# Optimization experiments

Hardware: AMD Instinct MI355X
Metric: run time of the kernel (lower is better)

The kernel has to match this reference:

```python
import jax, jax.numpy as jnp
import numpy as np

# NF4 codebook used by bitsandbytes Linear4bit (quant_type='nf4')
NF4_CODE = jnp.array([
    -1.0, -0.6961928009986877, -0.5250730514526367, -0.39491748809814453,
    -0.28444138169288635, -0.18477343022823334, -0.09105003625154495, 0.0,
    0.07958029955625534, 0.16093020141124725, 0.24611230194568634,
    0.33791524171829224, 0.44070982933044434, 0.5626170039176941,
    0.7229568362236023, 1.0], dtype=jnp.float32)

SCALE = 32.0 / 16.0  # alpha / r


def setup_inputs() -> dict:
    key = jax.random.key(0)
    k1, k2, k3, k4, k5 = jax.random.split(key, 5)
    B, S, IN, OUT, R = 4, 2048, 4096, 4096, 16
    BLK = 64  # Linear4bit default blocksize
    x = jax.random.normal(k1, (B, S, IN), dtype=jnp.float32)
    w_codes = jax.random.randint(k2, (OUT, IN), 0, 16, dtype=jnp.int32)
    absmax = jax.random.uniform(k3, (OUT, IN // BLK), dtype=jnp.float32)
    W_a = jax.random.normal(k4, (IN, R), dtype=jnp.float32)
    W_b = jax.random.normal(k5, (R, OUT), dtype=jnp.float32)
    return {"x": x, "w_codes": w_codes, "absmax": absmax, "W_a": W_a, "W_b": W_b}


def reference(x, w_codes, absmax, W_a, W_b):
    out_f, in_f = w_codes.shape
    blocks = absmax.shape[1]
    # NF4 dequantize: codebook lookup * per-block absmax scale  -> W [out, in]
    W = (NF4_CODE[w_codes].reshape(out_f, blocks, -1)
         * absmax[:, :, None]).reshape(out_f, in_f).astype(x.dtype)
    # quantized linear (no bias)
    y = jnp.einsum('bsi,oi->bso', x, W)
    # LoRA low-rank update: scale * (x @ W_a @ W_b)
    y = y + SCALE * ((x @ W_a.astype(x.dtype)) @ W_b.astype(x.dtype))
    return y
```

## Files before the change

### kernel.cpp

```cpp
#include <hip/hip_runtime.h>
#include <hip/hip_bf16.h>
#include <stdint.h>

#define IN_F 4096
#define OUT_F 4096
#define RANK 16
#define LORA_SCALE 2.0f

typedef __attribute__((ext_vector_type(8))) short short8;
typedef __attribute__((ext_vector_type(4))) float f32x4;
typedef __attribute__((ext_vector_type(16))) float f32x16;

__device__ __constant__ float NF4_CODE[16] = {
    -1.0f, -0.6961928009986877f, -0.5250730514526367f, -0.39491748809814453f,
    -0.28444138169288635f, -0.18477343022823334f, -0.09105003625154495f, 0.0f,
    0.07958029955625534f, 0.16093020141124725f, 0.24611230194568634f,
    0.33791524171829224f, 0.44070982933044434f, 0.5626170039176941f,
    0.7229568362236023f, 1.0f};

__device__ __forceinline__ short bf16_rne(float f) {
    uint32_t u = __builtin_bit_cast(uint32_t, f);
    u += 0x7fffu + ((u >> 16) & 1u);
    return (short)(u >> 16);
}

__device__ __forceinline__ void load_lds16(const short* g, short* l) {
    __builtin_amdgcn_global_load_lds(
        (const __attribute__((address_space(1))) void*)g,
        (__attribute__((address_space(3))) void*)l, 16, 0, 0);
}

__global__ __launch_bounds__(256)
void prep_kernel(const int* __restrict__ codes, const float* __restrict__ am,
                 const float* __restrict__ Wa, const float* __restrict__ Wb,
                 const float* __restrict__ x, short* __restrict__ Weff,
                 short* __restrict__ xb)
{
    const int tid = threadIdx.x;

    if (blockIdx.x >= 4096) {
        const size_t i = (size_t)(blockIdx.x - 4096) * 256 + tid;
        const f32x4* xv = (const f32x4*)x;
        f32x4 a = xv[2 * i], b = xv[2 * i + 1];
        short8 o;
        o[0] = bf16_rne(a[0]); o[1] = bf16_rne(a[1]);
        o[2] = bf16_rne(a[2]); o[3] = bf16_rne(a[3]);
        o[4] = bf16_rne(b[0]); o[5] = bf16_rne(b[1]);
        o[6] = bf16_rne(b[2]); o[7] = bf16_rne(b[3]);
        ((short8*)xb)[i] = o;
        return;
    }

    __shared__ float WaT[RANK * 64];
    __shared__ float Wbs[RANK * 64];

    const int iBase = (blockIdx.x & 63) * 64;
    const int oBase = (blockIdx.x >> 6) * 64;

    {
        f32x4 v = *(const f32x4*)(Wa + (size_t)iBase * RANK + tid * 4);
        #pragma unroll
        for (int j = 0; j < 4; j++) {
            int e = tid * 4 + j;
            WaT[(e & 15) * 64 + (e >> 4)] = v[j];
        }
        int r = tid >> 4, c = (tid & 15) * 4;
        f32x4 w = *(const f32x4*)(Wb + (size_t)r * OUT_F + oBase + c);
        *(f32x4*)&Wbs[r * 64 + c] = w;
    }
    __syncthreads();

    #pragma unroll
    for (int p = 0; p < 2; p++) {
        const int g  = tid + p * 256;
        const int o  = g >> 3;
        const int ig = (g & 7) * 8;
        const float amax = am[(size_t)(oBase + o) * (IN_F / 64) + (iBase >> 6)];

        const int4* cp = (const int4*)(codes + (size_t)(oBase + o) * IN_F + iBase + ig);
        int4 c0 = cp[0], c1 = cp[1];
        int cc[8] = {c0.x, c0.y, c0.z, c0.w, c1.x, c1.y, c1.z, c1.w};

        float acc[8] = {0, 0, 0, 0, 0, 0, 0, 0};
        #pragma unroll
        for (int r = 0; r < RANK; r++) {
            float wb = Wbs[r * 64 + o];
            f32x4 a0 = *(const f32x4*)&WaT[r * 64 + ig];
            f32x4 a1 = *(const f32x4*)&WaT[r * 64 + ig + 4];
            acc[0] += a0[0] * wb;  acc[1] += a0[1] * wb;
            acc[2] += a0[2] * wb;  acc[3] += a0[3] * wb;
            acc[4] += a1[0] * wb;  acc[5] += a1[1] * wb;
            acc[6] += a1[2] * wb;  acc[7] += a1[3] * wb;
        }

        short8 out;
        #pragma unroll
        for (int j = 0; j < 8; j++)
            out[j] = bf16_rne(NF4_CODE[cc[j] & 15] * amax + LORA_SCALE * acc[j]);
        *(short8*)(Weff + (size_t)(oBase + o) * IN_F + iBase + ig) = out;
    }
}

template<bool ABF16>
__global__ __launch_bounds__(256)
void gemm32(const void* __restrict__ Ain, const short* __restrict__ Bt,
            float* __restrict__ C)
{
    __shared__ __align__(16) short lds[16384];
    short* sA = lds;
    short* sB = lds + 8192;

    const int tid  = threadIdx.x;
    const int lane = tid & 63;
    const int wave = tid >> 6;
    const int mBase = blockIdx.y * 128;
    const int nBase = blockIdx.x * 128;
    const int wm = (wave >> 1) * 64;
    const int wn = (wave & 1) * 64;

    const int srow = tid >> 3;
    const int scol = ((tid & 7) ^ (srow & 7)) * 8;

    const short* gA[4]; const float* fA[4]; const short* gB[4];
    #pragma unroll
    for (int p = 0; p < 4; p++) {
        if constexpr (ABF16)
            gA[p] = (const short*)Ain + (size_t)(mBase + p * 32 + srow) * IN_F + scol;
        else
            fA[p] = (const float*)Ain + (size_t)(mBase + p * 32 + srow) * IN_F + scol;
        gB[p] = Bt + (size_t)(nBase + p * 32 + srow) * IN_F + scol;
    }
    short* dA[4]; short* dB[4];
    #pragma unroll
    for (int p = 0; p < 4; p++) {
        dA[p] = sA + (p * 256 + tid) * 8;
        dB[p] = sB + (p * 256 + tid) * 8;
    }

    const int l31 = lane & 31;
    const int h   = lane >> 5;
    const int r7  = lane & 7;
    int xo[4];
    #pragma unroll
    for (int s = 0; s < 4; s++) xo[s] = ((s * 2 + h) ^ r7) * 8;
    const int rA0 = (wm + l31) * 64, rA1 = rA0 + 32 * 64;
    const int rB0 = (wn + l31) * 64, rB1 = rB0 + 32 * 64;

    f32x16 acc[2][2];
    #pragma unroll
    for (int i = 0; i < 2; i++)
        #pragma unroll
        for (int j = 0; j < 2; j++)
            #pragma unroll
            for (int r = 0; r < 16; r++)
                acc[i][j][r] = 0.f;

    for (int k0 = 0; k0 < IN_F; k0 += 64) {
        if constexpr (ABF16) {
            #pragma unroll
            for (int p = 0; p < 4; p++) load_lds16(gA[p] + k0, dA[p]);
        } else {
            #pragma unroll
            for (int p = 0; p < 4; p++) {
                const float* s0 = fA[p] + k0;
                f32x4 v0 = *(const f32x4*)s0;
                f32x4 v1 = *(const f32x4*)(s0 + 4);
                short8 o;
                #pragma unroll
                for (int j = 0; j < 4; j++) {
                    o[j] = bf16_rne(v0[j]); o[j + 4] = bf16_rne(v1[j]);
                }
                *(short8*)dA[p] = o;
            }
        }
        #pragma unroll
        for (int p = 0; p < 4; p++) load_lds16(gB[p] + k0, dB[p]);
        __syncthreads();

        #pragma unroll
        for (int s = 0; s < 4; s++) {
            short8 a0 = *(const short8*)(sA + rA0 + xo[s]);
            short8 a1 = *(const short8*)(sA + rA1 + xo[s]);
            short8 b0 = *(const short8*)(sB + rB0 + xo[s]);
            short8 b1 = *(const short8*)(sB + rB1 + xo[s]);
            acc[0][0] = __builtin_amdgcn_mfma_f32_32x32x16_bf16(a0, b0, acc[0][0], 0, 0, 0);
            acc[0][1] = __builtin_amdgcn_mfma_f32_32x32x16_bf16(a0, b1, acc[0][1], 0, 0, 0);
            acc[1][0] = __builtin_amdgcn_mfma_f32_32x32x16_bf16(a1, b0, acc[1][0], 0, 0, 0);
            acc[1][1] = __builtin_amdgcn_mfma_f32_32x32x16_bf16(a1, b1, acc[1][1], 0, 0, 0);
        }
        __syncthreads();
    }

    #pragma unroll
    for (int mi = 0; mi < 2; mi++) {
        #pragma unroll
        for (int ni = 0; ni < 2; ni++) {
            const int col  = nBase + wn + ni * 32 + l31;
            const int rowb = mBase + wm + mi * 32 + 4 * h;
            #pragma unroll
            for (int r = 0; r < 16; r++) {
                const int row = rowb + (r & 3) + 8 * (r >> 2);
                C[(size_t)row * OUT_F + col] = acc[mi][ni][r];
            }
        }
    }
}

#define FENCE() __builtin_amdgcn_sched_barrier(0)
#define BARRIER() do { asm volatile("" ::: "memory"); FENCE(); \
    __builtin_amdgcn_s_barrier(); FENCE(); asm volatile("" ::: "memory"); } while(0)
#define WAIT_LGKM0() do { asm volatile("s_waitcnt lgkmcnt(0)" ::: "memory"); FENCE(); } while(0)
#define WAIT_VM6() do { asm volatile("s_waitcnt vmcnt(6)" ::: "memory"); FENCE(); } while(0)

#define STAGE_A(BUF, H, T) do { \
    const short* _g = gA + (size_t)(H) * 128 * IN_F + (T) * 64; \
    load_lds16(_g,                   lds + (BUF)*32768 + (H)*8192 + tid*8); \
    load_lds16(_g + (size_t)64*IN_F, lds + (BUF)*32768 + (H)*8192 + 4096 + tid*8); \
} while(0)

#define STAGE_B(BUF, H, T) do { \
    const short* _g = gB + (size_t)(H) * 128 * IN_F + (T) * 64; \
    load_lds16(_g,                   lds + (BUF)*32768 + 16384 + (H)*8192 + tid*8); \
    load_lds16(_g + (size_t)64*IN_F, lds + (BUF)*32768 + 16384 + (H)*8192 + 4096 + tid*8); \
} while(0)

#define READ_A(BUF, MQ) do { \
    const short* _s = lds + (BUF)*32768 + (MQ)*8192; \
    _Pragma("unroll") \
    for (int mf = 0; mf < 4; ++mf) { \
        const int row = wm*64 + mf*16 + l15; \
        const short* _r = _s + row*64; \
        const int rs = row & 7; \
        afr[mf][0] = *(const short8*)(_r + ((kl     ) ^ rs) * 8); \
        afr[mf][1] = *(const short8*)(_r + ((kl | 4) ^ rs) * 8); \
    } \
} while(0)

#define READ_B(BUF, NQ) do { \
    const short* _s = lds + (BUF)*32768 + 16384 + (NQ)*8192; \
    _Pragma("unroll") \
    for (int nf = 0; nf < 2; ++nf) { \
        const int row = wn*32 + nf*16 + l15; \
        const short* _r = _s + row*64; \
        const int rs = row & 7; \
        bfr[nf][0] = *(const short8*)(_r + ((kl     ) ^ rs) * 8); \
        bfr[nf][1] = *(const short8*)(_r + ((kl | 4) ^ rs) * 8); \
    } \
} while(0)

#define MFMA_QUAD(MQ, NQ) do { \
    _Pragma("unroll") \
    for (int ks = 0; ks < 2; ++ks) \
    _Pragma("unroll") \
    for (int mf = 0; mf < 4; ++mf) \
    _Pragma("unroll") \
    for (int nf = 0; nf < 2; ++nf) \
        acc[MQ][NQ][mf][nf] = __builtin_amdgcn_mfma_f32_16x16x32_bf16( \
            afr[mf][ks], bfr[nf][ks], acc[MQ][NQ][mf][nf], 0, 0, 0); \
} while(0)

#define PHASE(RDA, RDB, BUF, MQ, NQ, STAGE_STMT, VM_STMT) do { \
    if (RDA) READ_A(BUF, MQ); \
    if (RDB) READ_B(BUF, NQ); \
    STAGE_STMT; \
    BARRIER(); \
    WAIT_LGKM0(); \
    __builtin_amdgcn_s_setprio(1); \
    MFMA_QUAD(MQ, NQ); \
    __builtin_amdgcn_s_setprio(0); \
    VM_STMT; \
    BARRIER(); \
} while(0)

__global__ __launch_bounds__(512, 2)
void gemm256(const short* __restrict__ A, const short* __restrict__ Bt,
             float* __restrict__ C)
{
    __shared__ __align__(16) short lds[65536];

    const int tid  = threadIdx.x;
    const int lane = tid & 63;
    const int wave = tid >> 6;
    const int wm  = wave >> 2;
    const int wn  = wave & 3;
    const int l15 = lane & 15;
    const int kl  = lane >> 4;

    const int nwg = gridDim.x;
    int bid = blockIdx.x;
    bid = (bid & 7) * (nwg >> 3) + (bid >> 3);
    const int by = bid >> 4;
    const int bx = bid & 15;
    const int mBase = by * 256;
    const int nBase = bx * 256;

    const int rt = tid >> 3;
    const int sw = ((tid & 7) ^ (rt & 7)) * 8;
    const short* gA = A  + (size_t)(mBase + rt) * IN_F + sw;
    const short* gB = Bt + (size_t)(nBase + rt) * IN_F + sw;

    f32x4 acc[2][2][4][2];
    #pragma unroll
    for (int i = 0; i < 2; ++i)
    #pragma unroll
    for (int j = 0; j < 2; ++j)
    #pragma unroll
    for (int m = 0; m < 4; ++m)
    #pragma unroll
    for (int n = 0; n < 2; ++n)
    #pragma unroll
    for (int r = 0; r < 4; ++r)
        acc[i][j][m][n][r] = 0.f;

    short8 afr[4][2];
    short8 bfr[2][2];

    STAGE_A(0, 0, 0); STAGE_B(0, 1, 0); STAGE_A(0, 1, 0); STAGE_B(0, 0, 0);
    STAGE_A(1, 0, 1); STAGE_B(1, 1, 1); STAGE_A(1, 1, 1);
    WAIT_VM6();
    BARRIER();

    const int NT = IN_F / 64;
    #pragma unroll 1
    for (int it = 0; it < NT / 2; ++it) {
        const int T  = 2 * it;
        const int t2 = (T + 2 < NT) ? (T + 2) : (NT - 1);
        const int t3 = (T + 3 < NT) ? (T + 3) : (NT - 1);
        PHASE(1, 1, 0, 0, 0, STAGE_B(1, 0, T + 1), (void)0);
        PHASE(0, 1, 0, 0, 1, STAGE_A(0, 0, t2),    (void)0);
        PHASE(1, 0, 0, 1, 1, STAGE_B(0, 1, t2),    (void)0);
        PHASE(0, 1, 0, 1, 0, STAGE_A(0, 1, t2),    WAIT_VM6());
        PHASE(1, 1, 1, 0, 0, STAGE_B(0, 0, t2),    (void)0);
        PHASE(0, 1, 1, 0, 1, STAGE_A(1, 0, t3),    (void)0);
        PHASE(1, 0, 1, 1, 1, STAGE_B(1, 1, t3),    (void)0);
        PHASE(0, 1, 1, 1, 0, STAGE_A(1, 1, t3),    WAIT_VM6());
    }

    #pragma unroll
    for (int mq = 0; mq < 2; ++mq)
    #pragma unroll
    for (int nq = 0; nq < 2; ++nq)
    #pragma unroll
    for (int mf = 0; mf < 4; ++mf) {
        const int row0 = mBase + mq * 128 + wm * 64 + mf * 16 + kl * 4;
        #pragma unroll
        for (int nf = 0; nf < 2; ++nf) {
            const int col = nBase + nq * 128 + wn * 32 + nf * 16 + l15;
            float* cp = C + (size_t)row0 * OUT_F + col;
            #pragma unroll
            for (int r = 0; r < 4; ++r)
                cp[(size_t)r * OUT_F] = acc[mq][nq][mf][nf][r];
        }
    }
}

extern "C" void kernel_launch(void* const* d_in, const int* in_sizes, int n_in,
                              void* d_out, int out_size, void* d_ws, size_t ws_size,
                              hipStream_t stream)
{
    const float* x     = (const float*)d_in[0];
    const int*   codes = (const int*)d_in[1];
    const float* am    = (const float*)d_in[2];
    const float* Wa    = (const float*)d_in[3];
    const float* Wb    = (const float*)d_in[4];
    float* out = (float*)d_out;

    const int M = in_sizes[0] / IN_F;

    short* Weff = (short*)d_ws;
    short* xb   = Weff + (size_t)OUT_F * IN_F;
    const size_t need_full =
        ((size_t)OUT_F * IN_F + (size_t)M * IN_F) * sizeof(short);

    if (ws_size >= need_full) {
        const int castBlocks = (M * IN_F / 8) / 256;
        prep_kernel<<<4096 + castBlocks, 256, 0, stream>>>(
            codes, am, Wa, Wb, x, Weff, xb);
        if ((M & 255) == 0) {
            gemm256<<<dim3((OUT_F / 256) * (M / 256)), 512, 0, stream>>>(
                xb, Weff, out);
        } else {
            gemm32<true><<<dim3(OUT_F / 128, M / 128), 256, 0, stream>>>(
                xb, Weff, out);
        }
    } else {
        prep_kernel<<<4096, 256, 0, stream>>>(
            codes, am, Wa, Wb, x, Weff, Weff );
        gemm32<false><<<dim3(OUT_F / 128, M / 128), 256, 0, stream>>>(
            x, Weff, out);
    }
}
```

Before: 484.0 us.

## Split prep into weight and cast kernels; keep B fragments per N-quadrant in registers

Splits the combined prep kernel into a dedicated weight-merge kernel and a grid-stride x-cast kernel launched with a fixed grid. In the GEMM main loop, B fragments are now held per N quadrant, so two of the phases reuse the B fragments already in registers instead of reading them from LDS again. This cuts LDS read traffic in the GEMM at the cost of more VGPRs, which could affect occupancy at the launch bound of 2 blocks. The extra kernel launch adds a little overhead.

```diff
diff --git a/kernel.cpp b/kernel.cpp
--- a/kernel.cpp
+++ b/kernel.cpp
@@ -31,16 +31,69 @@
 }
 
 __global__ __launch_bounds__(256)
-void prep_kernel(const int* __restrict__ codes, const float* __restrict__ am,
+void weff_kernel(const int* __restrict__ codes, const float* __restrict__ am,
                  const float* __restrict__ Wa, const float* __restrict__ Wb,
-                 const float* __restrict__ x, short* __restrict__ Weff,
-                 short* __restrict__ xb)
+                 short* __restrict__ Weff)
 {
     const int tid = threadIdx.x;
 
-    if (blockIdx.x >= 4096) {
-        const size_t i = (size_t)(blockIdx.x - 4096) * 256 + tid;
-        const f32x4* xv = (const f32x4*)x;
+    __shared__ float WaT[RANK * 64];
+    __shared__ float Wbs[RANK * 64];
+
+    const int iBase = (blockIdx.x & 63) * 64;
+    const int oBase = (blockIdx.x >> 6) * 64;
+
+    {
+        f32x4 v = *(const f32x4*)(Wa + (size_t)iBase * RANK + tid * 4);
+        #pragma unroll
+        for (int j = 0; j < 4; j++) {
+            int e = tid * 4 + j;
+            WaT[(e & 15) * 64 + (e >> 4)] = v[j];
+        }
+        int r = tid >> 4, c = (tid & 15) * 4;
+        f32x4 w = *(const f32x4*)(Wb + (size_t)r * OUT_F + oBase + c);
+        *(f32x4*)&Wbs[r * 64 + c] = w;
+    }
+    __syncthreads();
+
+    #pragma unroll
+    for (int p = 0; p < 2; p++) {
+        const int g  = tid + p * 256;
+        const int o  = g >> 3;
+        const int ig = (g & 7) * 8;
+        const float amax = am[(size_t)(oBase + o) * (IN_F / 64) + (iBase >> 6)];
+
+        const int4* cp = (const int4*)(codes + (size_t)(oBase + o) * IN_F + iBase + ig);
+        int4 c0 = cp[0], c1 = cp[1];
+        int cc[8] = {c0.x, c0.y, c0.z, c0.w, c1.x, c1.y, c1.z, c1.w};
+
+        float acc[8] = {0, 0, 0, 0, 0, 0, 0, 0};
+        #pragma unroll
+        for (int r = 0; r < RANK; r++) {
+            float wb = Wbs[r * 64 + o];
+            f32x4 a0 = *(const f32x4*)&WaT[r * 64 + ig];
+            f32x4 a1 = *(const f32x4*)&WaT[r * 64 + ig + 4];
+            acc[0] += a0[0] * wb;  acc[1] += a0[1] * wb;
+            acc[2] += a0[2] * wb;  acc[3] += a0[3] * wb;
+            acc[4] += a1[0] * wb;  acc[5] += a1[1] * wb;
+            acc[6] += a1[2] * wb;  acc[7] += a1[3] * wb;
+        }
+
+        short8 out;
+        #pragma unroll
+        for (int j = 0; j < 8; j++)
+            out[j] = bf16_rne(NF4_CODE[cc[j] & 15] * amax + LORA_SCALE * acc[j]);
+        *(short8*)(Weff + (size_t)(oBase + o) * IN_F + iBase + ig) = out;
+    }
+}
+
+__global__ __launch_bounds__(256)
+void cast_x(const float* __restrict__ x, short* __restrict__ xb, int n8)
+{
+    int i = blockIdx.x * 256 + threadIdx.x;
+    const int stride = gridDim.x * 256;
+    const f32x4* xv = (const f32x4*)x;
+    for (; i < n8; i += stride) {
         f32x4 a = xv[2 * i], b = xv[2 * i + 1];
         short8 o;
         o[0] = bf16_rne(a[0]); o[1] = bf16_rne(a[1]);
@@ -48,8 +101,16 @@
         o[4] = bf16_rne(b[0]); o[5] = bf16_rne(b[1]);
         o[6] = bf16_rne(b[2]); o[7] = bf16_rne(b[3]);
         ((short8*)xb)[i] = o;
-        return;
-    }
+    }
+}
+
+__global__ __launch_bounds__(256)
+void prep_kernel(const int* __restrict__ codes, const float* __restrict__ am,
+                 const float* __restrict__ Wa, const float* __restrict__ Wb,
+                 const float* __restrict__ x, short* __restrict__ Weff,
+                 short* __restrict__ xb)
+{
+    const int tid = threadIdx.x;
 
     __shared__ float WaT[RANK * 64];
     __shared__ float Wbs[RANK * 64];
@@ -243,8 +304,8 @@
         const int row = wn*32 + nf*16 + l15; \
         const short* _r = _s + row*64; \
         const int rs = row & 7; \
-        bfr[nf][0] = *(const short8*)(_r + ((kl     ) ^ rs) * 8); \
-        bfr[nf][1] = *(const short8*)(_r + ((kl | 4) ^ rs) * 8); \
+        bfr[NQ][nf][0] = *(const short8*)(_r + ((kl     ) ^ rs) * 8); \
+        bfr[NQ][nf][1] = *(const short8*)(_r + ((kl | 4) ^ rs) * 8); \
     } \
 } while(0)
 
@@ -256,7 +317,7 @@
     _Pragma("unroll") \
     for (int nf = 0; nf < 2; ++nf) \
         acc[MQ][NQ][mf][nf] = __builtin_amdgcn_mfma_f32_16x16x32_bf16( \
-            afr[mf][ks], bfr[nf][ks], acc[MQ][NQ][mf][nf], 0, 0, 0); \
+            afr[mf][ks], bfr[NQ][nf][ks], acc[MQ][NQ][mf][nf], 0, 0, 0); \
 } while(0)
 
 #define PHASE(RDA, RDB, BUF, MQ, NQ, STAGE_STMT, VM_STMT) do { \
@@ -313,7 +374,7 @@
         acc[i][j][m][n][r] = 0.f;
 
     short8 afr[4][2];
-    short8 bfr[2][2];
+    short8 bfr[2][2][2];
 
     STAGE_A(0, 0, 0); STAGE_B(0, 1, 0); STAGE_A(0, 1, 0); STAGE_B(0, 0, 0);
     STAGE_A(1, 0, 1); STAGE_B(1, 1, 1); STAGE_A(1, 1, 1);
@@ -329,11 +390,11 @@
         PHASE(1, 1, 0, 0, 0, STAGE_B(1, 0, T + 1), (void)0);
         PHASE(0, 1, 0, 0, 1, STAGE_A(0, 0, t2),    (void)0);
         PHASE(1, 0, 0, 1, 1, STAGE_B(0, 1, t2),    (void)0);
-        PHASE(0, 1, 0, 1, 0, STAGE_A(0, 1, t2),    WAIT_VM6());
+        PHASE(0, 0, 0, 1, 0, STAGE_A(0, 1, t2),    WAIT_VM6());
         PHASE(1, 1, 1, 0, 0, STAGE_B(0, 0, t2),    (void)0);
         PHASE(0, 1, 1, 0, 1, STAGE_A(1, 0, t3),    (void)0);
         PHASE(1, 0, 1, 1, 1, STAGE_B(1, 1, t3),    (void)0);
-        PHASE(0, 1, 1, 1, 0, STAGE_A(1, 1, t3),    WAIT_VM6());
+        PHASE(0, 0, 1, 1, 0, STAGE_A(1, 1, t3),    WAIT_VM6());
     }
 
     #pragma unroll
@@ -373,9 +434,8 @@
         ((size_t)OUT_F * IN_F + (size_t)M * IN_F) * sizeof(short);
 
     if (ws_size >= need_full) {
-        const int castBlocks = (M * IN_F / 8) / 256;
-        prep_kernel<<<4096 + castBlocks, 256, 0, stream>>>(
-            codes, am, Wa, Wb, x, Weff, xb);
+        weff_kernel<<<4096, 256, 0, stream>>>(codes, am, Wa, Wb, Weff);
+        cast_x<<<2048, 256, 0, stream>>>(x, xb, M * IN_F / 8);
         if ((M & 255) == 0) {
             gemm256<<<dim3((OUT_F / 256) * (M / 256)), 512, 0, stream>>>(
                 xb, Weff, out);
```

New measurement: 490.2 us. Within noise of the previous version (+1.3%).
